# Performance work log

Measured on AMD Instinct MI355X. Metric: run time of the kernel, lower is better.

## Reference

```python
import jax, jax.numpy as jnp
import numpy as np

B, S, H, R = 32, 512, 1024, 64


def _bernoulli(key, shape, p=0.05):
    return (jax.random.uniform(key, shape) < p).astype(jnp.float32)


def setup_inputs() -> dict:
    key = jax.random.key(0)
    ks = jax.random.split(key, 16)
    context = jax.random.normal(ks[0], (B, S, H), dtype=jnp.float32)
    masks = jnp.ones((B, S), dtype=jnp.float32)
    all_subject_heads = _bernoulli(ks[1], (B, S))
    all_subject_tails = _bernoulli(ks[2], (B, S))
    # one-hot subject head/tail positions (tail >= head)
    h_pos = jax.random.randint(ks[3], (B,), 0, S // 2)
    t_pos = h_pos + jax.random.randint(ks[4], (B,), 0, 8)
    subject_head = jax.nn.one_hot(h_pos, S, dtype=jnp.float32)
    subject_tail = jax.nn.one_hot(t_pos, S, dtype=jnp.float32)
    object_heads = _bernoulli(ks[5], (B, S, R))
    object_tails = _bernoulli(ks[6], (B, S, R))
    # learned parameters (PyTorch Linear: y = x @ W.T + b; store as [in, out])
    sc = 1.0 / np.sqrt(H)
    Ws_h = jax.random.uniform(ks[7], (H, 1), minval=-sc, maxval=sc)
    bs_h = jnp.zeros((1,), dtype=jnp.float32)
    Ws_t = jax.random.uniform(ks[8], (H, 1), minval=-sc, maxval=sc)
    bs_t = jnp.zeros((1,), dtype=jnp.float32)
    Wo_h = jax.random.uniform(ks[9], (H, R), minval=-sc, maxval=sc)
    bo_h = jnp.zeros((R,), dtype=jnp.float32)
    Wo_t = jax.random.uniform(ks[10], (H, R), minval=-sc, maxval=sc)
    bo_t = jnp.zeros((R,), dtype=jnp.float32)
    return dict(context=context, masks=masks,
                all_subject_heads=all_subject_heads, all_subject_tails=all_subject_tails,
                subject_head=subject_head, subject_tail=subject_tail,
                object_heads=object_heads, object_tails=object_tails,
                Ws_h=Ws_h, bs_h=bs_h, Ws_t=Ws_t, bs_t=bs_t,
                Wo_h=Wo_h, bo_h=bo_h, Wo_t=Wo_t, bo_t=bo_t)


def _bce_with_logits(logits, targets):
    # numerically stable, matches F.binary_cross_entropy_with_logits(reduction='none')
    return jnp.maximum(logits, 0.0) - logits * targets + jnp.log1p(jnp.exp(-jnp.abs(logits)))


def _masked_loss(gold, pred, mask):
    loss = _bce_with_logits(pred, gold)
    if loss.ndim != mask.ndim:
        mask = mask[..., None]
    return jnp.sum(loss * mask) / jnp.sum(mask)


def reference(context, masks, all_subject_heads, all_subject_tails,
              subject_head, subject_tail, object_heads, object_tails,
              Ws_h, bs_h, Ws_t, bs_t, Wo_h, bo_h, Wo_t, bo_t):
    # subject logits: [B,S]
    pred_subject_heads = (context @ Ws_h + bs_h)[..., 0]
    pred_subject_tails = (context @ Ws_t + bs_t)[..., 0]
    # subject pooling: one-hot [B,S] x context [B,S,H] -> [B,H]
    sub_h = jnp.einsum('bs,bsh->bh', subject_head, context)
    sub_t = jnp.einsum('bs,bsh->bh', subject_tail, context)
    subject = (sub_h + sub_t) * 0.5
    context_subject = context + subject[:, None, :]  # [B,S,H]
    pred_object_heads = context_subject @ Wo_h + bo_h  # [B,S,R]
    pred_object_tails = context_subject @ Wo_t + bo_t  # [B,S,R]
    loss = (_masked_loss(all_subject_heads, pred_subject_heads, masks)
            + _masked_loss(all_subject_tails, pred_subject_tails, masks)
            + _masked_loss(object_heads, pred_object_heads, masks)
            + _masked_loss(object_tails, pred_object_tails, masks))
    return loss
```

## Files before the change

kernel.cpp:

```cpp
#include <hip/hip_runtime.h>


#define B_  32
#define S_  512
#define H_  1024
#define R_  64
#define M_  (B_ * S_)
#define NPAD 160
#define NVALID 130

typedef __attribute__((ext_vector_type(4))) float  floatx4;
typedef __attribute__((ext_vector_type(8))) short  short8;

__device__ __forceinline__ unsigned short f2bf(float f) {
    unsigned int u = __float_as_uint(f);
    u = (u + 0x7FFFu + ((u >> 16) & 1u)) >> 16;
    return (unsigned short)u;
}

__global__ __launch_bounds__(256) void prep_kernel(
        const float* __restrict__ ctx,  const float* __restrict__ head,
        const float* __restrict__ tail,
        const float* __restrict__ Ws_h, const float* __restrict__ Ws_t,
        const float* __restrict__ Wo_h, const float* __restrict__ Wo_t,
        const float* __restrict__ bo_h, const float* __restrict__ bo_t,
        const float* __restrict__ bs_h, const float* __restrict__ bs_t,
        unsigned short* __restrict__ WtG, float* __restrict__ rowBias) {
    const int blk = blockIdx.x, tid = threadIdx.x;
    if (blk < NPAD) {
        const int n = blk;
        for (int k = tid; k < H_; k += 256) {
            float v;
            if (n < 64)        v = Wo_h[k * R_ + n];
            else if (n < 128)  v = Wo_t[k * R_ + (n - 64)];
            else if (n == 128) v = Ws_h[k];
            else if (n == 129) v = Ws_t[k];
            else               v = 0.0f;
            WtG[n * H_ + k] = f2bf(v);
        }
        return;
    }
    const int b = blk - NPAD;
    __shared__ float subj[H_];
    __shared__ float part[256];
    __shared__ int cnt;
    __shared__ int   sidx[4];
    __shared__ float sw[4];
    if (tid == 0) cnt = 0;
    __syncthreads();
    for (int s = tid; s < S_; s += 256) {
        float w = 0.5f * (head[b * S_ + s] + tail[b * S_ + s]);
        if (w != 0.0f) {
            int i = atomicAdd(&cnt, 1);
            if (i < 4) { sidx[i] = s; sw[i] = w; }
        }
    }
    __syncthreads();
    const int nnz = cnt < 4 ? cnt : 4;
    for (int h = tid; h < H_; h += 256) {
        float a = 0.0f;
        for (int i = 0; i < nnz; i++)
            a += sw[i] * ctx[((size_t)b * S_ + sidx[i]) * H_ + h];
        subj[h] = a;
    }
    __syncthreads();
    {
        const int c = tid & 127, hf = tid >> 7;
        const float* W = (c < 64) ? (Wo_h + c) : (Wo_t + (c - 64));
        float a = 0.0f;
        const int k0 = hf * 512;
#pragma unroll 8
        for (int k = k0; k < k0 + 512; k++)
            a += subj[k] * W[(size_t)k * R_];
        part[tid] = a;
    }
    __syncthreads();
    if (tid < NPAD) {
        float v;
        if (tid < 128)
            v = part[tid] + part[128 + tid] + (tid < 64 ? bo_h[tid] : bo_t[tid - 64]);
        else if (tid == 128) v = bs_h[0];
        else if (tid == 129) v = bs_t[0];
        else                 v = 0.0f;
        rowBias[b * NPAD + tid] = v;
    }
}

__global__ __launch_bounds__(256) void main_kernel(
        const float* __restrict__ ctx, const unsigned short* __restrict__ WtG,
        const float* __restrict__ rowBias, const float* __restrict__ masks,
        const float* __restrict__ ash, const float* __restrict__ ast,
        const float* __restrict__ oh, const float* __restrict__ ot,
        float* __restrict__ accum) {
    __shared__ float rbuf[4];
    const int tid  = threadIdx.x;
    const int gm0  = blockIdx.x * 32;
    const int b    = gm0 >> 9;
    const int wave = tid >> 6, lane = tid & 63;
    const int wm = wave & 1;
    const int wn = wave >> 1;
    const int lr = lane & 15, q = lane >> 4;

    if (tid < 32) {
        float mv = masks[gm0 + tid];
#pragma unroll
        for (int o = 16; o > 0; o >>= 1) mv += __shfl_down(mv, o, 64);
        if (tid == 0) atomicAdd(&accum[1], mv);
    }

    const float* aP = ctx + (size_t)(gm0 + wm * 16 + lr) * H_ + q * 8;
    const unsigned short* bB[5];
#pragma unroll
    for (int t = 0; t < 5; t++)
        bB[t] = WtG + (size_t)(wn * 80 + t * 16 + lr) * H_ + q * 8;

    floatx4 acc[5];
#pragma unroll
    for (int t = 0; t < 5; t++) acc[t] = (floatx4){0.f, 0.f, 0.f, 0.f};

    float4 a0[2], a1[2];
    short8 bv[2][5];
    a0[0] = *(const float4*)(aP + 0);
    a1[0] = *(const float4*)(aP + 4);
#pragma unroll
    for (int t = 0; t < 5; t++) bv[0][t] = *(const short8*)(bB[t] + 0);

#pragma unroll
    for (int i = 0; i < 32; i++) {
        const int cur = i & 1, nxt = cur ^ 1;
        if (i < 31) {
            const int k = (i + 1) * 32;
            a0[nxt] = *(const float4*)(aP + k);
            a1[nxt] = *(const float4*)(aP + k + 4);
#pragma unroll
            for (int t = 0; t < 5; t++) bv[nxt][t] = *(const short8*)(bB[t] + k);
        }
        short8 af;
        af[0] = (short)f2bf(a0[cur].x); af[1] = (short)f2bf(a0[cur].y);
        af[2] = (short)f2bf(a0[cur].z); af[3] = (short)f2bf(a0[cur].w);
        af[4] = (short)f2bf(a1[cur].x); af[5] = (short)f2bf(a1[cur].y);
        af[6] = (short)f2bf(a1[cur].z); af[7] = (short)f2bf(a1[cur].w);
#pragma unroll
        for (int t = 0; t < 5; t++)
            acc[t] = __builtin_amdgcn_mfma_f32_16x16x32_bf16(af, bv[cur][t], acc[t], 0, 0, 0);
    }

    float lsum = 0.0f;
#pragma unroll
    for (int t = 0; t < 5; t++) {
        const int col = wn * 80 + t * 16 + lr;
        if (col < NVALID) {
            const float rb = rowBias[b * NPAD + col];
#pragma unroll
            for (int i = 0; i < 4; i++) {
                const int row = gm0 + wm * 16 + q * 4 + i;
                const float l = acc[t][i] + rb;
                float tgt;
                if (col < 64)        tgt = oh[row * R_ + col];
                else if (col < 128)  tgt = ot[row * R_ + (col - 64)];
                else if (col == 128) tgt = ash[row];
                else                 tgt = ast[row];
                const float mk = masks[row];
                const float bce = fmaxf(l, 0.0f) - l * tgt + log1pf(__expf(-fabsf(l)));
                lsum += bce * mk;
            }
        }
    }
#pragma unroll
    for (int o = 32; o > 0; o >>= 1) lsum += __shfl_down(lsum, o, 64);
    if (lane == 0) rbuf[wave] = lsum;
    __syncthreads();
    if (tid == 0) atomicAdd(&accum[0], rbuf[0] + rbuf[1] + rbuf[2] + rbuf[3]);
}

__global__ void finalize_kernel(const float* __restrict__ accum, float* __restrict__ out) {
    out[0] = accum[0] / accum[1];
}

extern "C" void kernel_launch(void* const* d_in, const int* in_sizes, int n_in,
                              void* d_out, int out_size, void* d_ws, size_t ws_size,
                              hipStream_t stream) {
    const float* ctx   = (const float*)d_in[0];
    const float* masks = (const float*)d_in[1];
    const float* ash   = (const float*)d_in[2];
    const float* ast   = (const float*)d_in[3];
    const float* sh    = (const float*)d_in[4];
    const float* st    = (const float*)d_in[5];
    const float* oh    = (const float*)d_in[6];
    const float* ot    = (const float*)d_in[7];
    const float* Ws_h  = (const float*)d_in[8];
    const float* Ws_t  = (const float*)d_in[10];
    const float* bs_h  = (const float*)d_in[9];
    const float* bs_t  = (const float*)d_in[11];
    const float* Wo_h  = (const float*)d_in[12];
    const float* bo_h  = (const float*)d_in[13];
    const float* Wo_t  = (const float*)d_in[14];
    const float* bo_t  = (const float*)d_in[15];
    float* out = (float*)d_out;

    char* ws = (char*)d_ws;
    float* accum   = (float*)(ws + 0);
    float* rowBias = (float*)(ws + 256);
    unsigned short* WtG = (unsigned short*)(ws + 256 + 32 * NPAD * 4);

    hipMemsetAsync(accum, 0, 8, stream);
    prep_kernel<<<NPAD + B_, 256, 0, stream>>>(ctx, sh, st, Ws_h, Ws_t,
                                               Wo_h, Wo_t, bo_h, bo_t, bs_h, bs_t,
                                               WtG, rowBias);
    main_kernel<<<M_ / 32, 256, 0, stream>>>(ctx, WtG, rowBias, masks,
                                             ash, ast, oh, ot, accum);
    finalize_kernel<<<1, 1, 0, stream>>>(accum, out);
}
```

Measured before the change: 194.6 us.

## Split-K GEMM across waves with tiled weight layout and fused finalize

The main kernel now assigns each block a 16-row by 80-column tile and splits the K=1024 reduction across its four waves, combining the partial accumulators through shared memory before the BCE epilogue. Weights are stored K-block-major so each wave's B-operand loads are contiguous. The memset and finalize kernel are removed: prep zeroes the accumulators and a ticket counter, and the last main block writes the result. This removes launches and adds parallelism, but each context row is now read by two blocks and an extra LDS reduction and barrier are added.

```diff
diff --git a/kernel.cpp b/kernel.cpp
--- a/kernel.cpp
+++ b/kernel.cpp
@@ -8,6 +8,7 @@
 #define M_  (B_ * S_)
 #define NPAD 160
 #define NVALID 130
+#define NBLK (M_ / 16 * 2)
 
 typedef __attribute__((ext_vector_type(4))) float  floatx4;
 typedef __attribute__((ext_vector_type(8))) short  short8;
@@ -25,8 +26,13 @@
         const float* __restrict__ Wo_h, const float* __restrict__ Wo_t,
         const float* __restrict__ bo_h, const float* __restrict__ bo_t,
         const float* __restrict__ bs_h, const float* __restrict__ bs_t,
-        unsigned short* __restrict__ WtG, float* __restrict__ rowBias) {
+        unsigned short* __restrict__ Wt3, float* __restrict__ rowBias,
+        float* __restrict__ accum, int* __restrict__ ticket) {
     const int blk = blockIdx.x, tid = threadIdx.x;
+    if (blk == 0) {
+        if (tid < 2) accum[tid] = 0.0f;
+        if (tid == 2) *ticket = 0;
+    }
     if (blk < NPAD) {
         const int n = blk;
         for (int k = tid; k < H_; k += 256) {
@@ -36,7 +42,7 @@
             else if (n == 128) v = Ws_h[k];
             else if (n == 129) v = Ws_t[k];
             else               v = 0.0f;
-            WtG[n * H_ + k] = f2bf(v);
+            Wt3[(k >> 5) * (NPAD * 32) + n * 32 + (k & 31)] = f2bf(v);
         }
         return;
     }
@@ -69,7 +75,7 @@
         const float* W = (c < 64) ? (Wo_h + c) : (Wo_t + (c - 64));
         float a = 0.0f;
         const int k0 = hf * 512;
-#pragma unroll 8
+#pragma unroll 16
         for (int k = k0; k < k0 + 512; k++)
             a += subj[k] * W[(size_t)k * R_];
         part[tid] = a;
@@ -86,95 +92,100 @@
     }
 }
 
-__global__ __launch_bounds__(256) void main_kernel(
-        const float* __restrict__ ctx, const unsigned short* __restrict__ WtG,
+__global__ __launch_bounds__(256, 8) void main_kernel(
+        const float* __restrict__ ctx, const unsigned short* __restrict__ Wt3,
         const float* __restrict__ rowBias, const float* __restrict__ masks,
         const float* __restrict__ ash, const float* __restrict__ ast,
         const float* __restrict__ oh, const float* __restrict__ ot,
-        float* __restrict__ accum) {
-    __shared__ float rbuf[4];
+        float* __restrict__ accum, int* __restrict__ ticket,
+        float* __restrict__ out) {
+    __shared__ float red[3][64][21];
     const int tid  = threadIdx.x;
-    const int gm0  = blockIdx.x * 32;
-    const int b    = gm0 >> 9;
     const int wave = tid >> 6, lane = tid & 63;
-    const int wm = wave & 1;
-    const int wn = wave >> 1;
     const int lr = lane & 15, q = lane >> 4;
-
-    if (tid < 32) {
-        float mv = masks[gm0 + tid];
-#pragma unroll
-        for (int o = 16; o > 0; o >>= 1) mv += __shfl_down(mv, o, 64);
-        if (tid == 0) atomicAdd(&accum[1], mv);
-    }
-
-    const float* aP = ctx + (size_t)(gm0 + wm * 16 + lr) * H_ + q * 8;
-    const unsigned short* bB[5];
-#pragma unroll
-    for (int t = 0; t < 5; t++)
-        bB[t] = WtG + (size_t)(wn * 80 + t * 16 + lr) * H_ + q * 8;
+    const int wn  = blockIdx.x & 1;
+    const int gm0 = (blockIdx.x >> 1) << 4;
+    const int b   = gm0 >> 9;
+    const int k0  = wave << 8;
+
+    const float* aP = ctx + (size_t)(gm0 + lr) * H_ + k0 + q * 8;
+    const unsigned short* bP = Wt3 + (size_t)(k0 >> 5) * (NPAD * 32)
+                               + (wn * 80 + 32 + lr) * 32 + q * 8;
 
     floatx4 acc[5];
 #pragma unroll
     for (int t = 0; t < 5; t++) acc[t] = (floatx4){0.f, 0.f, 0.f, 0.f};
 
-    float4 a0[2], a1[2];
-    short8 bv[2][5];
-    a0[0] = *(const float4*)(aP + 0);
-    a1[0] = *(const float4*)(aP + 4);
-#pragma unroll
-    for (int t = 0; t < 5; t++) bv[0][t] = *(const short8*)(bB[t] + 0);
-
-#pragma unroll
-    for (int i = 0; i < 32; i++) {
-        const int cur = i & 1, nxt = cur ^ 1;
-        if (i < 31) {
-            const int k = (i + 1) * 32;
-            a0[nxt] = *(const float4*)(aP + k);
-            a1[nxt] = *(const float4*)(aP + k + 4);
-#pragma unroll
-            for (int t = 0; t < 5; t++) bv[nxt][t] = *(const short8*)(bB[t] + k);
-        }
+#pragma unroll
+    for (int it = 0; it < 8; ++it) {
+        const float4 a0 = *(const float4*)(aP + it * 32);
+        const float4 a1 = *(const float4*)(aP + it * 32 + 4);
+        short8 bv[5];
+#pragma unroll
+        for (int t = 0; t < 5; t++)
+            bv[t] = *(const short8*)(bP + (t - 2) * 512);
+        bP += NPAD * 32;
         short8 af;
-        af[0] = (short)f2bf(a0[cur].x); af[1] = (short)f2bf(a0[cur].y);
-        af[2] = (short)f2bf(a0[cur].z); af[3] = (short)f2bf(a0[cur].w);
-        af[4] = (short)f2bf(a1[cur].x); af[5] = (short)f2bf(a1[cur].y);
-        af[6] = (short)f2bf(a1[cur].z); af[7] = (short)f2bf(a1[cur].w);
+        af[0] = (short)f2bf(a0.x); af[1] = (short)f2bf(a0.y);
+        af[2] = (short)f2bf(a0.z); af[3] = (short)f2bf(a0.w);
+        af[4] = (short)f2bf(a1.x); af[5] = (short)f2bf(a1.y);
+        af[6] = (short)f2bf(a1.z); af[7] = (short)f2bf(a1.w);
 #pragma unroll
         for (int t = 0; t < 5; t++)
-            acc[t] = __builtin_amdgcn_mfma_f32_16x16x32_bf16(af, bv[cur][t], acc[t], 0, 0, 0);
-    }
-
-    float lsum = 0.0f;
-#pragma unroll
-    for (int t = 0; t < 5; t++) {
-        const int col = wn * 80 + t * 16 + lr;
-        if (col < NVALID) {
-            const float rb = rowBias[b * NPAD + col];
+            acc[t] = __builtin_amdgcn_mfma_f32_16x16x32_bf16(af, bv[t], acc[t], 0, 0, 0);
+    }
+
+    if (wave != 0) {
+#pragma unroll
+        for (int t = 0; t < 5; t++)
+#pragma unroll
+            for (int i = 0; i < 4; i++)
+                red[wave - 1][lane][t * 4 + i] = acc[t][i];
+    }
+    if (wn == 0 && wave == 1 && lane < 16) {
+        float mv = masks[gm0 + lane];
+#pragma unroll
+        for (int o = 8; o > 0; o >>= 1) mv += __shfl_down(mv, o, 64);
+        if (lane == 0) atomicAdd(&accum[1], mv);
+    }
+    __syncthreads();
+    if (wave == 0) {
+        float lsum = 0.0f;
+#pragma unroll
+        for (int t = 0; t < 5; t++) {
+            const int col = wn * 80 + t * 16 + lr;
 #pragma unroll
             for (int i = 0; i < 4; i++) {
-                const int row = gm0 + wm * 16 + q * 4 + i;
-                const float l = acc[t][i] + rb;
-                float tgt;
-                if (col < 64)        tgt = oh[row * R_ + col];
-                else if (col < 128)  tgt = ot[row * R_ + (col - 64)];
-                else if (col == 128) tgt = ash[row];
-                else                 tgt = ast[row];
-                const float mk = masks[row];
-                const float bce = fmaxf(l, 0.0f) - l * tgt + log1pf(__expf(-fabsf(l)));
-                lsum += bce * mk;
+                const float v = acc[t][i] + red[0][lane][t * 4 + i]
+                              + red[1][lane][t * 4 + i] + red[2][lane][t * 4 + i];
+                if (col < NVALID) {
+                    const int row = gm0 + q * 4 + i;
+                    const float l = v + rowBias[b * NPAD + col];
+                    float tgt;
+                    if (col < 64)        tgt = oh[row * R_ + col];
+                    else if (col < 128)  tgt = ot[row * R_ + (col - 64)];
+                    else if (col == 128) tgt = ash[row];
+                    else                 tgt = ast[row];
+                    const float bce = fmaxf(l, 0.0f) - l * tgt
+                                    + log1pf(__expf(-fabsf(l)));
+                    lsum += bce * masks[row];
+                }
             }
         }
-    }
-#pragma unroll
-    for (int o = 32; o > 0; o >>= 1) lsum += __shfl_down(lsum, o, 64);
-    if (lane == 0) rbuf[wave] = lsum;
-    __syncthreads();
-    if (tid == 0) atomicAdd(&accum[0], rbuf[0] + rbuf[1] + rbuf[2] + rbuf[3]);
-}
-
-__global__ void finalize_kernel(const float* __restrict__ accum, float* __restrict__ out) {
-    out[0] = accum[0] / accum[1];
+#pragma unroll
+        for (int o = 32; o > 0; o >>= 1) lsum += __shfl_down(lsum, o, 64);
+        if (lane == 0) atomicAdd(&accum[0], lsum);
+    }
+    __syncthreads();
+    if (tid == 0) {
+        __threadfence();
+        const int old = atomicAdd(ticket, 1);
+        if (old == NBLK - 1) {
+            const float s = atomicAdd(&accum[0], 0.0f);
+            const float m = atomicAdd(&accum[1], 0.0f);
+            out[0] = s / m;
+        }
+    }
 }
 
 extern "C" void kernel_launch(void* const* d_in, const int* in_sizes, int n_in,
@@ -189,8 +200,8 @@
     const float* oh    = (const float*)d_in[6];
     const float* ot    = (const float*)d_in[7];
     const float* Ws_h  = (const float*)d_in[8];
+    const float* bs_h  = (const float*)d_in[9];
     const float* Ws_t  = (const float*)d_in[10];
-    const float* bs_h  = (const float*)d_in[9];
     const float* bs_t  = (const float*)d_in[11];
     const float* Wo_h  = (const float*)d_in[12];
     const float* bo_h  = (const float*)d_in[13];
@@ -200,14 +211,13 @@
 
     char* ws = (char*)d_ws;
     float* accum   = (float*)(ws + 0);
+    int*   ticket  = (int*)(ws + 64);
     float* rowBias = (float*)(ws + 256);
-    unsigned short* WtG = (unsigned short*)(ws + 256 + 32 * NPAD * 4);
-
-    hipMemsetAsync(accum, 0, 8, stream);
+    unsigned short* Wt3 = (unsigned short*)(ws + 256 + 32 * NPAD * 4);
+
     prep_kernel<<<NPAD + B_, 256, 0, stream>>>(ctx, sh, st, Ws_h, Ws_t,
                                                Wo_h, Wo_t, bo_h, bo_t, bs_h, bs_t,
-                                               WtG, rowBias);
-    main_kernel<<<M_ / 32, 256, 0, stream>>>(ctx, WtG, rowBias, masks,
-                                             ash, ast, oh, ot, accum);
-    finalize_kernel<<<1, 1, 0, stream>>>(accum, out);
-}
+                                               Wt3, rowBias, accum, ticket);
+    main_kernel<<<NBLK, 256, 0, stream>>>(ctx, Wt3, rowBias, masks,
+                                          ash, ast, oh, ot, accum, ticket, out);
+}
```

Result: slower. 229.8 us (+18.1%).
